# Kernel optimization log

Hardware: AMD Instinct MI355X
Metric: run time of the kernel (lower is better)

Reference implementation:

```python
import jax, jax.numpy as jnp
import numpy as np

N = 50000      # nodes
E = 1600000    # edges (avg degree 32)
R = 8          # relation types
G = 64         # graphs in batch
D_IN = 128
HID = 128
CLS = 10


def setup_inputs() -> dict:
    key = jax.random.key(0)
    ks = jax.random.split(key, 12)
    s = 0.05  # weight init scale
    return {
        "x": jax.random.normal(ks[0], (N, D_IN), dtype=jnp.float32),
        "edge_index": jax.random.randint(ks[1], (2, E), 0, N, dtype=jnp.int32),
        "edge_type": jax.random.randint(ks[2], (E,), 0, R, dtype=jnp.int32),
        "batch": jnp.sort(jax.random.randint(ks[3], (N,), 0, G, dtype=jnp.int32)),
        "W1": jax.random.normal(ks[4], (R, D_IN, HID), dtype=jnp.float32) * s,
        "root1": jax.random.normal(ks[5], (D_IN, HID), dtype=jnp.float32) * s,
        "b1": jax.random.normal(ks[6], (HID,), dtype=jnp.float32) * s,
        "W2": jax.random.normal(ks[7], (R, HID, HID), dtype=jnp.float32) * s,
        "root2": jax.random.normal(ks[8], (HID, HID), dtype=jnp.float32) * s,
        "b2": jax.random.normal(ks[9], (HID,), dtype=jnp.float32) * s,
        "lin_w": jax.random.normal(ks[10], (HID, CLS), dtype=jnp.float32) * s,
        "lin_b": jax.random.normal(ks[11], (CLS,), dtype=jnp.float32) * s,
    }


def rgcn_conv(x, edge_index, edge_type, W, root, bias):
    # PyG RGCNConv (default aggr='mean'): per-relation mean of neighbor
    # features, relation-specific matmul, summed over relations, + root + bias.
    src, dst = edge_index[0], edge_index[1]
    d_in = x.shape[1]
    seg = dst * R + edge_type                      # fused (node, relation) segment id
    msg = jax.ops.segment_sum(x[src], seg, num_segments=N * R)          # [N*R, d_in]
    cnt = jax.ops.segment_sum(jnp.ones((E,), x.dtype), seg, num_segments=N * R)
    mean = (msg / jnp.maximum(cnt, 1.0)[:, None]).reshape(N, R, d_in)   # [N, R, d_in]
    return jnp.einsum('nrd,rdh->nh', mean, W) + x @ root + bias


def reference(x, edge_index, edge_type, batch, W1, root1, b1, W2, root2, b2, lin_w, lin_b):
    h = jax.nn.relu(rgcn_conv(x, edge_index, edge_type, W1, root1, b1))
    h = jax.nn.relu(rgcn_conv(h, edge_index, edge_type, W2, root2, b2))
    # global mean pool per graph
    gsum = jax.ops.segment_sum(h, batch, num_segments=G)                # [G, HID]
    gcnt = jax.ops.segment_sum(jnp.ones((N,), h.dtype), batch, num_segments=G)
    g = gsum / jnp.maximum(gcnt, 1.0)[:, None]
    return g @ lin_w + lin_b                                            # [G, CLS]
```

## Files before the change

kernel.cpp:

```cpp
#include <hip/hip_runtime.h>

#define N_NODES 50000
#define N_EDGES 1600000
#define R_REL 8
#define G_GRAPHS 64
#define D_INF 128
#define HIDF 128
#define CLSF 10

#define S_SEG (N_NODES * R_REL)
#define RZ 9
#define PCHUNK 16

#define XG 8
#define NODES_PER_G (N_NODES / XG)
#define SEGS_PER_G (NODES_PER_G * R_REL)
#define SORT_BLKS_PER_G 256
#define SORT_GRID (XG * SORT_BLKS_PER_G)

typedef __attribute__((ext_vector_type(8))) short short8;
typedef __attribute__((ext_vector_type(4))) float floatx4;
typedef __attribute__((ext_vector_type(2))) float f32x2;

typedef __attribute__((address_space(1))) const unsigned int guint;
typedef __attribute__((address_space(3))) unsigned int luint;
__device__ __forceinline__ void gload_lds16(const void* g, void* l) {
    __builtin_amdgcn_global_load_lds((guint*)g, (luint*)l, 16, 0, 0);
}

__device__ __forceinline__ unsigned short f2bf(float f) {
    unsigned int u = __float_as_uint(f);
    unsigned int r = (u + 0x7fffu + ((u >> 16) & 1u)) >> 16;
    return (unsigned short)r;
}
__device__ __forceinline__ float bflo(unsigned int u) { return __uint_as_float(u << 16); }
__device__ __forceinline__ float bfhi(unsigned int u) { return __uint_as_float(u & 0xffff0000u); }
__device__ __forceinline__ f32x2 bfpair(unsigned int u) {
    return (f32x2){__uint_as_float(u << 16), __uint_as_float(u & 0xffff0000u)};
}

__device__ __forceinline__ int ntload(const int* p) { return __builtin_nontemporal_load(p); }

__global__ __launch_bounds__(256) void seg_kernel(const int* __restrict__ dst,
                                                  const int* __restrict__ et,
                                                  int* __restrict__ seg) {
    int i4 = blockIdx.x * 256 + threadIdx.x;
    if (i4 * 4 >= N_EDGES) return;
    int4 d = ((const int4*)dst)[i4];
    int4 t = ((const int4*)et)[i4];
    int4 s;
    s.x = d.x * R_REL + t.x; s.y = d.y * R_REL + t.y;
    s.z = d.z * R_REL + t.z; s.w = d.w * R_REL + t.w;
    ((int4*)seg)[i4] = s;
}

__global__ __launch_bounds__(256) void count_kernel(const int* __restrict__ seg,
                                                    int* __restrict__ cnt,
                                                    unsigned short* __restrict__ rank) {
    int xg = blockIdx.x & (XG - 1);
    int inner = blockIdx.x >> 3;
    int lo = xg * SEGS_PER_G, hi = lo + SEGS_PER_G;
    for (int e = inner * 256 + threadIdx.x; e < N_EDGES; e += SORT_BLKS_PER_G * 256) {
        int sg = ntload(seg + e);
        if (sg >= lo && sg < hi)
            rank[e] = (unsigned short)atomicAdd(&cnt[sg], 1);
    }
}

#define SCAN_BLK 256
#define SCAN_ELEMS 1024
#define NB_SCAN ((S_SEG + SCAN_ELEMS - 1) / SCAN_ELEMS)

__global__ __launch_bounds__(SCAN_BLK) void scan1_kernel(const int* __restrict__ cnt,
                                                         int* __restrict__ off,
                                                         int* __restrict__ bsum) {
    __shared__ int sd[SCAN_BLK];
    int t = threadIdx.x;
    int base = blockIdx.x * SCAN_ELEMS + t * 4;
    int v[4];
    int tsum = 0;
#pragma unroll
    for (int j = 0; j < 4; j++) {
        v[j] = (base + j < S_SEG) ? cnt[base + j] : 0;
        tsum += v[j];
    }
    sd[t] = tsum;
    __syncthreads();
    for (int d = 1; d < SCAN_BLK; d <<= 1) {
        int x = (t >= d) ? sd[t - d] : 0;
        __syncthreads();
        sd[t] += x;
        __syncthreads();
    }
    int incl = sd[t];
    int run = incl - tsum;
#pragma unroll
    for (int j = 0; j < 4; j++) {
        if (base + j < S_SEG) off[base + j] = run;
        run += v[j];
    }
    if (t == SCAN_BLK - 1) bsum[blockIdx.x] = incl;
}

__global__ __launch_bounds__(512) void absoff2_kernel(int* __restrict__ off,
                                                      const int* __restrict__ bsum) {
    __shared__ int sd[512];
    int t = threadIdx.x;
    int v = (t < NB_SCAN) ? bsum[t] : 0;
    sd[t] = v;
    __syncthreads();
    for (int d = 1; d < 512; d <<= 1) {
        int x = (t >= d) ? sd[t - d] : 0;
        __syncthreads();
        sd[t] += x;
        __syncthreads();
    }
    int pre = (blockIdx.x == 0) ? 0 : sd[blockIdx.x - 1];
    int base = blockIdx.x * SCAN_ELEMS + t * 2;
#pragma unroll
    for (int j = 0; j < 2; j++) {
        int i = base + j;
        if (i < S_SEG) off[i] += pre;
    }
}

__global__ __launch_bounds__(256) void scatter_kernel(const int* __restrict__ seg,
                                                      const int* __restrict__ src,
                                                      const unsigned short* __restrict__ rank,
                                                      const int* __restrict__ off,
                                                      unsigned short* __restrict__ esrc) {
    int i4 = blockIdx.x * 256 + threadIdx.x;
    if (i4 * 4 >= N_EDGES) return;
    int4 s4 = ((const int4*)seg)[i4];
    int4 r4 = ((const int4*)src)[i4];
    ushort4 k4 = ((const ushort4*)rank)[i4];
    esrc[off[s4.x] + k4.x] = (unsigned short)r4.x;
    esrc[off[s4.y] + k4.y] = (unsigned short)r4.y;
    esrc[off[s4.z] + k4.z] = (unsigned short)r4.z;
    esrc[off[s4.w] + k4.w] = (unsigned short)r4.w;
}

__global__ void convx_kernel(const float* __restrict__ x, unsigned short* __restrict__ xb) {
    int idx = blockIdx.x * blockDim.x + threadIdx.x;
    if (idx < N_NODES * D_INF) xb[idx] = f2bf(x[idx]);
}

__global__ __launch_bounds__(256) void convw9_kernel(const float* __restrict__ W,
                                                     const float* __restrict__ root,
                                                     unsigned short* __restrict__ wz) {
    __shared__ float t[16][17];
    int r = blockIdx.z;
    int k0 = blockIdx.x * 16, c0 = blockIdx.y * 16;
    int tx = threadIdx.x & 15, ty = threadIdx.x >> 4;
    const float* srcp = (r < 8) ? (W + (size_t)r * 128 * 128) : root;
    t[ty][tx] = srcp[(size_t)(k0 + ty) * 128 + c0 + tx];
    __syncthreads();
    wz[(size_t)r * 16384 + (size_t)(c0 + ty) * 128 + k0 + tx] = f2bf(t[tx][ty]);
}

__global__ __launch_bounds__(256) void agg_mean(
    const unsigned short* __restrict__ hsrc,
    const unsigned short* __restrict__ esrc,
    const int* __restrict__ off,
    unsigned short* __restrict__ m)
{
    int sg = blockIdx.x * 16 + (threadIdx.x >> 4);
    int l = threadIdx.x & 15;
    int beg = off[sg];
    int end = (sg + 1 < S_SEG) ? off[sg + 1] : N_EDGES;
    float w = 1.0f / (float)max(end - beg, 1);

    f32x2 p0 = (f32x2){0.f, 0.f}, p1 = (f32x2){0.f, 0.f};
    f32x2 p2 = (f32x2){0.f, 0.f}, p3 = (f32x2){0.f, 0.f};
    int e = beg;
    for (; e + 4 <= end; e += 4) {
        int s0 = esrc[e], s1 = esrc[e + 1], s2 = esrc[e + 2], s3 = esrc[e + 3];
        uint4 v0 = *(const uint4*)(hsrc + (size_t)s0 * HIDF + l * 8);
        uint4 v1 = *(const uint4*)(hsrc + (size_t)s1 * HIDF + l * 8);
        uint4 v2 = *(const uint4*)(hsrc + (size_t)s2 * HIDF + l * 8);
        uint4 v3 = *(const uint4*)(hsrc + (size_t)s3 * HIDF + l * 8);
        p0 += bfpair(v0.x) + bfpair(v1.x) + bfpair(v2.x) + bfpair(v3.x);
        p1 += bfpair(v0.y) + bfpair(v1.y) + bfpair(v2.y) + bfpair(v3.y);
        p2 += bfpair(v0.z) + bfpair(v1.z) + bfpair(v2.z) + bfpair(v3.z);
        p3 += bfpair(v0.w) + bfpair(v1.w) + bfpair(v2.w) + bfpair(v3.w);
    }
    for (; e < end; e++) {
        int s0 = esrc[e];
        uint4 v0 = *(const uint4*)(hsrc + (size_t)s0 * HIDF + l * 8);
        p0 += bfpair(v0.x); p1 += bfpair(v0.y);
        p2 += bfpair(v0.z); p3 += bfpair(v0.w);
    }
    uint4 o;
    o.x = (unsigned int)f2bf(p0.x * w) | ((unsigned int)f2bf(p0.y * w) << 16);
    o.y = (unsigned int)f2bf(p1.x * w) | ((unsigned int)f2bf(p1.y * w) << 16);
    o.z = (unsigned int)f2bf(p2.x * w) | ((unsigned int)f2bf(p2.y * w) << 16);
    o.w = (unsigned int)f2bf(p3.x * w) | ((unsigned int)f2bf(p3.y * w) << 16);
    *(uint4*)(m + (size_t)sg * HIDF + l * 8) = o;
}

__global__ __launch_bounds__(256) void transform9(
    const unsigned short* __restrict__ mm,
    const unsigned short* __restrict__ hsrc,
    const unsigned short* __restrict__ wz,
    const float* __restrict__ bias,
    unsigned short* __restrict__ hout)
{
    __shared__ __align__(16) unsigned short A4[4][128][32];
    __shared__ __align__(16) unsigned short B4[4][128][32];

    const int tx = threadIdx.x;
    const int wave = tx >> 6, lane = tx & 63;
    const int quad = lane >> 4, lq = lane & 15;
    const int srow = lane >> 2, sch = lane & 3;
    const int row0 = blockIdx.x * 128;

    floatx4 acc[2][8];
#pragma unroll
    for (int i = 0; i < 2; i++)
#pragma unroll
        for (int j = 0; j < 8; j++) acc[i][j] = (floatx4){0.f, 0.f, 0.f, 0.f};

    for (int r = 0; r < RZ; r++) {
#pragma unroll
        for (int kk = 0; kk < 4; kk++) {
#pragma unroll
            for (int p = 0; p < 2; p++) {
                int rr = (wave * 2 + p) * 16;
                int gr = row0 + rr + srow; if (gr >= N_NODES) gr = N_NODES - 1;
                const unsigned short* ap = (r < 8)
                    ? mm + (size_t)gr * (R_REL * HIDF) + r * HIDF
                    : hsrc + (size_t)gr * HIDF;
                gload_lds16(ap + kk * 32 + sch * 8, &A4[kk][rr][0]);
                gload_lds16(wz + ((size_t)r * 128 + rr + srow) * 128 + kk * 32 + sch * 8,
                            &B4[kk][rr][0]);
            }
        }
        __syncthreads();

#pragma unroll
        for (int kk = 0; kk < 4; kk++) {
            short8 af[2], bfr[8];
#pragma unroll
            for (int i = 0; i < 2; i++)
                af[i] = *(const short8*)(&A4[kk][wave * 32 + i * 16 + lq][quad * 8]);
#pragma unroll
            for (int j = 0; j < 8; j++)
                bfr[j] = *(const short8*)(&B4[kk][j * 16 + lq][quad * 8]);
#pragma unroll
            for (int i = 0; i < 2; i++)
#pragma unroll
                for (int j = 0; j < 8; j++)
                    acc[i][j] = __builtin_amdgcn_mfma_f32_16x16x32_bf16(af[i], bfr[j], acc[i][j], 0, 0, 0);
        }
        __syncthreads();
    }

#pragma unroll
    for (int i = 0; i < 2; i++)
#pragma unroll
        for (int j = 0; j < 8; j++) {
            int col = j * 16 + lq;
            float bv = bias[col];
#pragma unroll
            for (int rg = 0; rg < 4; rg++) {
                int row = row0 + wave * 32 + i * 16 + quad * 4 + rg;
                if (row < N_NODES)
                    hout[(size_t)row * HIDF + col] = f2bf(fmaxf(acc[i][j][rg] + bv, 0.f));
            }
        }
}

__global__ __launch_bounds__(256) void pool1_kernel(const unsigned short* __restrict__ h,
                                                    const int* __restrict__ batch,
                                                    float* __restrict__ partial) {
    int g = blockIdx.x;
    int p = blockIdx.y;
    int lo, hi;
    {
        int l = 0, r = N_NODES;
        while (l < r) { int m = (l + r) >> 1; if (batch[m] < g) l = m + 1; else r = m; }
        lo = l;
        l = lo; r = N_NODES;
        while (l < r) { int m = (l + r) >> 1; if (batch[m] < g + 1) l = m + 1; else r = m; }
        hi = l;
    }
    int t = threadIdx.x;
    int rowlane = t >> 5;
    int c4 = t & 31;
    float a0 = 0.f, a1 = 0.f, a2 = 0.f, a3 = 0.f;
    for (int n = lo + p + rowlane * PCHUNK; n < hi; n += 8 * PCHUNK) {
        uint2 v = *(const uint2*)(h + (size_t)n * HIDF + c4 * 4);
        a0 += bflo(v.x); a1 += bfhi(v.x); a2 += bflo(v.y); a3 += bfhi(v.y);
    }
    __shared__ float red[8][128];
    if (rowlane == 0) {
        red[0][c4 * 4 + 0] = a0; red[0][c4 * 4 + 1] = a1;
        red[0][c4 * 4 + 2] = a2; red[0][c4 * 4 + 3] = a3;
    }
    __syncthreads();
    for (int s = 1; s < 8; s++) {
        if (rowlane == s) {
            red[0][c4 * 4 + 0] += a0; red[0][c4 * 4 + 1] += a1;
            red[0][c4 * 4 + 2] += a2; red[0][c4 * 4 + 3] += a3;
        }
        __syncthreads();
    }
    if (t < 128) partial[((size_t)g * PCHUNK + p) * 128 + t] = red[0][t];
}

__global__ __launch_bounds__(128) void poolfin_kernel(const float* __restrict__ partial,
                                                      const int* __restrict__ batch,
                                                      const float* __restrict__ lin_w,
                                                      const float* __restrict__ lin_b,
                                                      float* __restrict__ out) {
    __shared__ float gl[HIDF];
    int g = blockIdx.x;
    int lo, hi;
    {
        int l = 0, r = N_NODES;
        while (l < r) { int m = (l + r) >> 1; if (batch[m] < g) l = m + 1; else r = m; }
        lo = l;
        l = lo; r = N_NODES;
        while (l < r) { int m = (l + r) >> 1; if (batch[m] < g + 1) l = m + 1; else r = m; }
        hi = l;
    }
    int t = threadIdx.x;
    float s = 0.f;
#pragma unroll
    for (int p = 0; p < PCHUNK; p++)
        s += partial[((size_t)g * PCHUNK + p) * 128 + t];
    gl[t] = s / (float)max(hi - lo, 1);
    __syncthreads();
    if (t < CLSF) {
        float acc = lin_b[t];
#pragma unroll 16
        for (int d = 0; d < HIDF; d++) acc += gl[d] * lin_w[d * CLSF + t];
        out[g * CLSF + t] = acc;
    }
}

extern "C" void kernel_launch(void* const* d_in, const int* in_sizes, int n_in,
                              void* d_out, int out_size, void* d_ws, size_t ws_size,
                              hipStream_t stream) {
    const float* x     = (const float*)d_in[0];
    const int*   ei    = (const int*)d_in[1];
    const int*   et    = (const int*)d_in[2];
    const int*   batch = (const int*)d_in[3];
    const float* W1    = (const float*)d_in[4];
    const float* root1 = (const float*)d_in[5];
    const float* b1    = (const float*)d_in[6];
    const float* W2    = (const float*)d_in[7];
    const float* root2 = (const float*)d_in[8];
    const float* b2    = (const float*)d_in[9];
    const float* lin_w = (const float*)d_in[10];
    const float* lin_b = (const float*)d_in[11];
    float* out = (float*)d_out;

    const int* src = ei;
    const int* dst = ei + N_EDGES;

    char* ws = (char*)d_ws;
    unsigned short* xb  = (unsigned short*)ws; ws += (size_t)N_NODES * HIDF * 2;
    unsigned short* h1  = (unsigned short*)ws; ws += (size_t)N_NODES * HIDF * 2;
    unsigned short* h2  = (unsigned short*)ws; ws += (size_t)N_NODES * HIDF * 2;
    unsigned short* m   = (unsigned short*)ws; ws += (size_t)S_SEG * HIDF * 2;
    unsigned short* wz1 = (unsigned short*)ws; ws += (size_t)RZ * 128 * 128 * 2;
    unsigned short* wz2 = (unsigned short*)ws; ws += (size_t)RZ * 128 * 128 * 2;
    int*   seg    = (int*)ws;   ws += (size_t)N_EDGES * 4;
    int*   cnt    = (int*)ws;   ws += (size_t)S_SEG * 4;
    int*   off    = (int*)ws;   ws += (size_t)S_SEG * 4;
    int*   bsum   = (int*)ws;   ws += 512 * 4;
    unsigned short* rank = (unsigned short*)ws; ws += (size_t)N_EDGES * 2;
    unsigned short* esrc = (unsigned short*)ws; ws += (size_t)N_EDGES * 2;
    float* partial = (float*)ws; ws += (size_t)G_GRAPHS * PCHUNK * 128 * 4;

    hipMemsetAsync(cnt, 0, (size_t)S_SEG * 4, stream);

    seg_kernel<<<(N_EDGES / 4 + 255) / 256, 256, 0, stream>>>(dst, et, seg);
    count_kernel<<<SORT_GRID, 256, 0, stream>>>(seg, cnt, rank);
    scan1_kernel<<<NB_SCAN, SCAN_BLK, 0, stream>>>(cnt, off, bsum);
    absoff2_kernel<<<NB_SCAN, 512, 0, stream>>>(off, bsum);
    scatter_kernel<<<(N_EDGES / 4 + 255) / 256, 256, 0, stream>>>(seg, src, rank, off, esrc);

    convx_kernel<<<(N_NODES * D_INF + 255) / 256, 256, 0, stream>>>(x, xb);
    convw9_kernel<<<dim3(8, 8, RZ), 256, 0, stream>>>(W1, root1, wz1);
    convw9_kernel<<<dim3(8, 8, RZ), 256, 0, stream>>>(W2, root2, wz2);

    const int NGB = (N_NODES + 127) / 128;
    const int NSB = S_SEG / 16;

    agg_mean<<<NSB, 256, 0, stream>>>(xb, esrc, off, m);
    transform9<<<NGB, 256, 0, stream>>>(m, xb, wz1, b1, h1);

    agg_mean<<<NSB, 256, 0, stream>>>(h1, esrc, off, m);
    transform9<<<NGB, 256, 0, stream>>>(m, h1, wz2, b2, h2);

    pool1_kernel<<<dim3(G_GRAPHS, PCHUNK), 256, 0, stream>>>(h2, batch, partial);
    poolfin_kernel<<<G_GRAPHS, 128, 0, stream>>>(partial, batch, lin_w, lin_b, out);

    (void)in_sizes; (void)n_in; (void)out_size; (void)ws_size;
}
```

Before: 430.2 us.

## Fuse mean aggregation into MFMA relation transform, drop intermediate buffer

Replaces the separate agg_mean and transform9 kernels with a single fused kernel. Each lane gathers and averages neighbour rows for its node and relation directly into MFMA A-fragments in registers, so the N*R*128 bf16 intermediate is never written to or read back from global memory. The cost is a different parallel mapping: each lane now walks a whole segment over 4 k-chunks, giving less parallelism per segment and more register pressure, with each wave handling 16 nodes instead of 32. The x to bf16 conversion kernel is also vectorised to float4 loads.

```diff
diff --git a/kernel.cpp b/kernel.cpp
--- a/kernel.cpp
+++ b/kernel.cpp
@@ -37,6 +37,14 @@
 __device__ __forceinline__ float bfhi(unsigned int u) { return __uint_as_float(u & 0xffff0000u); }
 __device__ __forceinline__ f32x2 bfpair(unsigned int u) {
     return (f32x2){__uint_as_float(u << 16), __uint_as_float(u & 0xffff0000u)};
+}
+__device__ __forceinline__ short8 pack8(f32x2 a, f32x2 b, f32x2 c, f32x2 d, float w) {
+    union { uint4 u; short8 s; } o;
+    o.u.x = (unsigned int)f2bf(a.x * w) | ((unsigned int)f2bf(a.y * w) << 16);
+    o.u.y = (unsigned int)f2bf(b.x * w) | ((unsigned int)f2bf(b.y * w) << 16);
+    o.u.z = (unsigned int)f2bf(c.x * w) | ((unsigned int)f2bf(c.y * w) << 16);
+    o.u.w = (unsigned int)f2bf(d.x * w) | ((unsigned int)f2bf(d.y * w) << 16);
+    return o.s;
 }
 
 __device__ __forceinline__ int ntload(const int* p) { return __builtin_nontemporal_load(p); }
@@ -140,9 +148,15 @@
     esrc[off[s4.w] + k4.w] = (unsigned short)r4.w;
 }
 
-__global__ void convx_kernel(const float* __restrict__ x, unsigned short* __restrict__ xb) {
-    int idx = blockIdx.x * blockDim.x + threadIdx.x;
-    if (idx < N_NODES * D_INF) xb[idx] = f2bf(x[idx]);
+__global__ __launch_bounds__(256) void convx_kernel(const float* __restrict__ x,
+                                                    unsigned short* __restrict__ xb) {
+    int i4 = blockIdx.x * 256 + threadIdx.x;
+    if (i4 * 4 < N_NODES * D_INF) {
+        float4 v = ((const float4*)x)[i4];
+        ushort4 o;
+        o.x = f2bf(v.x); o.y = f2bf(v.y); o.z = f2bf(v.z); o.w = f2bf(v.w);
+        ((ushort4*)xb)[i4] = o;
+    }
 }
 
 __global__ __launch_bounds__(256) void convw9_kernel(const float* __restrict__ W,
@@ -158,116 +172,112 @@
     wz[(size_t)r * 16384 + (size_t)(c0 + ty) * 128 + k0 + tx] = f2bf(t[tx][ty]);
 }
 
-__global__ __launch_bounds__(256) void agg_mean(
+__global__ __launch_bounds__(256, 3) void fused_rt(
     const unsigned short* __restrict__ hsrc,
     const unsigned short* __restrict__ esrc,
     const int* __restrict__ off,
-    unsigned short* __restrict__ m)
-{
-    int sg = blockIdx.x * 16 + (threadIdx.x >> 4);
-    int l = threadIdx.x & 15;
-    int beg = off[sg];
-    int end = (sg + 1 < S_SEG) ? off[sg + 1] : N_EDGES;
-    float w = 1.0f / (float)max(end - beg, 1);
-
-    f32x2 p0 = (f32x2){0.f, 0.f}, p1 = (f32x2){0.f, 0.f};
-    f32x2 p2 = (f32x2){0.f, 0.f}, p3 = (f32x2){0.f, 0.f};
-    int e = beg;
-    for (; e + 4 <= end; e += 4) {
-        int s0 = esrc[e], s1 = esrc[e + 1], s2 = esrc[e + 2], s3 = esrc[e + 3];
-        uint4 v0 = *(const uint4*)(hsrc + (size_t)s0 * HIDF + l * 8);
-        uint4 v1 = *(const uint4*)(hsrc + (size_t)s1 * HIDF + l * 8);
-        uint4 v2 = *(const uint4*)(hsrc + (size_t)s2 * HIDF + l * 8);
-        uint4 v3 = *(const uint4*)(hsrc + (size_t)s3 * HIDF + l * 8);
-        p0 += bfpair(v0.x) + bfpair(v1.x) + bfpair(v2.x) + bfpair(v3.x);
-        p1 += bfpair(v0.y) + bfpair(v1.y) + bfpair(v2.y) + bfpair(v3.y);
-        p2 += bfpair(v0.z) + bfpair(v1.z) + bfpair(v2.z) + bfpair(v3.z);
-        p3 += bfpair(v0.w) + bfpair(v1.w) + bfpair(v2.w) + bfpair(v3.w);
-    }
-    for (; e < end; e++) {
-        int s0 = esrc[e];
-        uint4 v0 = *(const uint4*)(hsrc + (size_t)s0 * HIDF + l * 8);
-        p0 += bfpair(v0.x); p1 += bfpair(v0.y);
-        p2 += bfpair(v0.z); p3 += bfpair(v0.w);
-    }
-    uint4 o;
-    o.x = (unsigned int)f2bf(p0.x * w) | ((unsigned int)f2bf(p0.y * w) << 16);
-    o.y = (unsigned int)f2bf(p1.x * w) | ((unsigned int)f2bf(p1.y * w) << 16);
-    o.z = (unsigned int)f2bf(p2.x * w) | ((unsigned int)f2bf(p2.y * w) << 16);
-    o.w = (unsigned int)f2bf(p3.x * w) | ((unsigned int)f2bf(p3.y * w) << 16);
-    *(uint4*)(m + (size_t)sg * HIDF + l * 8) = o;
-}
-
-__global__ __launch_bounds__(256) void transform9(
-    const unsigned short* __restrict__ mm,
-    const unsigned short* __restrict__ hsrc,
     const unsigned short* __restrict__ wz,
     const float* __restrict__ bias,
     unsigned short* __restrict__ hout)
 {
-    __shared__ __align__(16) unsigned short A4[4][128][32];
     __shared__ __align__(16) unsigned short B4[4][128][32];
 
     const int tx = threadIdx.x;
     const int wave = tx >> 6, lane = tx & 63;
     const int quad = lane >> 4, lq = lane & 15;
     const int srow = lane >> 2, sch = lane & 3;
-    const int row0 = blockIdx.x * 128;
-
-    floatx4 acc[2][8];
-#pragma unroll
-    for (int i = 0; i < 2; i++)
-#pragma unroll
-        for (int j = 0; j < 8; j++) acc[i][j] = (floatx4){0.f, 0.f, 0.f, 0.f};
+    const int node0 = blockIdx.x * 64 + wave * 16;
+    const bool wvalid = (node0 < N_NODES);
+    const int node = node0 + lq;
+
+    floatx4 acc[8];
+#pragma unroll
+    for (int j = 0; j < 8; j++) acc[j] = (floatx4){0.f, 0.f, 0.f, 0.f};
 
     for (int r = 0; r < RZ; r++) {
 #pragma unroll
-        for (int kk = 0; kk < 4; kk++) {
+        for (int kk = 0; kk < 4; kk++)
 #pragma unroll
             for (int p = 0; p < 2; p++) {
                 int rr = (wave * 2 + p) * 16;
-                int gr = row0 + rr + srow; if (gr >= N_NODES) gr = N_NODES - 1;
-                const unsigned short* ap = (r < 8)
-                    ? mm + (size_t)gr * (R_REL * HIDF) + r * HIDF
-                    : hsrc + (size_t)gr * HIDF;
-                gload_lds16(ap + kk * 32 + sch * 8, &A4[kk][rr][0]);
                 gload_lds16(wz + ((size_t)r * 128 + rr + srow) * 128 + kk * 32 + sch * 8,
                             &B4[kk][rr][0]);
             }
+
+        short8 af[4];
+        if (wvalid) {
+            if (r < 8) {
+                int sg = node * R_REL + r;
+                int beg = off[sg];
+                int end = (sg + 1 < S_SEG) ? off[sg + 1] : N_EDGES;
+                float w = 1.0f / (float)max(end - beg, 1);
+                f32x2 pa[16];
+#pragma unroll
+                for (int i = 0; i < 16; i++) pa[i] = (f32x2){0.f, 0.f};
+                const unsigned short* hq = hsrc + quad * 8;
+                int e = beg;
+                for (; e + 2 <= end; e += 2) {
+                    int s0 = esrc[e], s1 = esrc[e + 1];
+                    const unsigned short* r0 = hq + (size_t)s0 * HIDF;
+                    const unsigned short* r1 = hq + (size_t)s1 * HIDF;
+#pragma unroll
+                    for (int kk = 0; kk < 4; kk++) {
+                        uint4 v0 = *(const uint4*)(r0 + kk * 32);
+                        uint4 v1 = *(const uint4*)(r1 + kk * 32);
+                        pa[kk * 4 + 0] += bfpair(v0.x) + bfpair(v1.x);
+                        pa[kk * 4 + 1] += bfpair(v0.y) + bfpair(v1.y);
+                        pa[kk * 4 + 2] += bfpair(v0.z) + bfpair(v1.z);
+                        pa[kk * 4 + 3] += bfpair(v0.w) + bfpair(v1.w);
+                    }
+                }
+                if (e < end) {
+                    int s0 = esrc[e];
+                    const unsigned short* r0 = hq + (size_t)s0 * HIDF;
+#pragma unroll
+                    for (int kk = 0; kk < 4; kk++) {
+                        uint4 v0 = *(const uint4*)(r0 + kk * 32);
+                        pa[kk * 4 + 0] += bfpair(v0.x);
+                        pa[kk * 4 + 1] += bfpair(v0.y);
+                        pa[kk * 4 + 2] += bfpair(v0.z);
+                        pa[kk * 4 + 3] += bfpair(v0.w);
+                    }
+                }
+#pragma unroll
+                for (int kk = 0; kk < 4; kk++)
+                    af[kk] = pack8(pa[kk * 4 + 0], pa[kk * 4 + 1],
+                                   pa[kk * 4 + 2], pa[kk * 4 + 3], w);
+            } else {
+#pragma unroll
+                for (int kk = 0; kk < 4; kk++)
+                    af[kk] = *(const short8*)(hsrc + (size_t)node * HIDF + quad * 8 + kk * 32);
+            }
         }
         __syncthreads();
 
-#pragma unroll
-        for (int kk = 0; kk < 4; kk++) {
-            short8 af[2], bfr[8];
-#pragma unroll
-            for (int i = 0; i < 2; i++)
-                af[i] = *(const short8*)(&A4[kk][wave * 32 + i * 16 + lq][quad * 8]);
-#pragma unroll
-            for (int j = 0; j < 8; j++)
-                bfr[j] = *(const short8*)(&B4[kk][j * 16 + lq][quad * 8]);
-#pragma unroll
-            for (int i = 0; i < 2; i++)
-#pragma unroll
-                for (int j = 0; j < 8; j++)
-                    acc[i][j] = __builtin_amdgcn_mfma_f32_16x16x32_bf16(af[i], bfr[j], acc[i][j], 0, 0, 0);
+        if (wvalid) {
+#pragma unroll
+            for (int kk = 0; kk < 4; kk++)
+#pragma unroll
+                for (int j = 0; j < 8; j++) {
+                    short8 b = *(const short8*)(&B4[kk][j * 16 + lq][quad * 8]);
+                    acc[j] = __builtin_amdgcn_mfma_f32_16x16x32_bf16(af[kk], b, acc[j], 0, 0, 0);
+                }
         }
         __syncthreads();
     }
 
-#pragma unroll
-    for (int i = 0; i < 2; i++)
+    if (wvalid) {
 #pragma unroll
         for (int j = 0; j < 8; j++) {
             int col = j * 16 + lq;
             float bv = bias[col];
 #pragma unroll
             for (int rg = 0; rg < 4; rg++) {
-                int row = row0 + wave * 32 + i * 16 + quad * 4 + rg;
-                if (row < N_NODES)
-                    hout[(size_t)row * HIDF + col] = f2bf(fmaxf(acc[i][j][rg] + bv, 0.f));
+                int row = node0 + quad * 4 + rg;
+                hout[(size_t)row * HIDF + col] = f2bf(fmaxf(acc[j][rg] + bv, 0.f));
             }
         }
+    }
 }
 
 __global__ __launch_bounds__(256) void pool1_kernel(const unsigned short* __restrict__ h,
@@ -363,7 +373,6 @@
     unsigned short* xb  = (unsigned short*)ws; ws += (size_t)N_NODES * HIDF * 2;
     unsigned short* h1  = (unsigned short*)ws; ws += (size_t)N_NODES * HIDF * 2;
     unsigned short* h2  = (unsigned short*)ws; ws += (size_t)N_NODES * HIDF * 2;
-    unsigned short* m   = (unsigned short*)ws; ws += (size_t)S_SEG * HIDF * 2;
     unsigned short* wz1 = (unsigned short*)ws; ws += (size_t)RZ * 128 * 128 * 2;
     unsigned short* wz2 = (unsigned short*)ws; ws += (size_t)RZ * 128 * 128 * 2;
     int*   seg    = (int*)ws;   ws += (size_t)N_EDGES * 4;
@@ -382,18 +391,14 @@
     absoff2_kernel<<<NB_SCAN, 512, 0, stream>>>(off, bsum);
     scatter_kernel<<<(N_EDGES / 4 + 255) / 256, 256, 0, stream>>>(seg, src, rank, off, esrc);
 
-    convx_kernel<<<(N_NODES * D_INF + 255) / 256, 256, 0, stream>>>(x, xb);
+    convx_kernel<<<(N_NODES * D_INF / 4 + 255) / 256, 256, 0, stream>>>(x, xb);
     convw9_kernel<<<dim3(8, 8, RZ), 256, 0, stream>>>(W1, root1, wz1);
     convw9_kernel<<<dim3(8, 8, RZ), 256, 0, stream>>>(W2, root2, wz2);
 
-    const int NGB = (N_NODES + 127) / 128;
-    const int NSB = S_SEG / 16;
-
-    agg_mean<<<NSB, 256, 0, stream>>>(xb, esrc, off, m);
-    transform9<<<NGB, 256, 0, stream>>>(m, xb, wz1, b1, h1);
-
-    agg_mean<<<NSB, 256, 0, stream>>>(h1, esrc, off, m);
-    transform9<<<NGB, 256, 0, stream>>>(m, h1, wz2, b2, h2);
+    const int NFB = (N_NODES + 63) / 64;
+
+    fused_rt<<<NFB, 256, 0, stream>>>(xb, esrc, off, wz1, b1, h1);
+    fused_rt<<<NFB, 256, 0, stream>>>(h1, esrc, off, wz2, b2, h2);
 
     pool1_kernel<<<dim3(G_GRAPHS, PCHUNK), 256, 0, stream>>>(h2, batch, partial);
     poolfin_kernel<<<G_GRAPHS, 128, 0, stream>>>(partial, batch, lin_w, lin_b, out);
```

New measurement: 471.9 us. 1.1x slower.
